# Kernel tuning notes

Measured on AMD Instinct MI355X. Metric: run time of the kernel, lower is better.

## Reference

```python
import jax, jax.numpy as jnp
import numpy as np

H = 12          # num heads
D = 768         # embed dim
HD = D // H     # head dim
SCALE = HD ** -0.5
NEG = -(3.0 ** 39)  # matches torch's triu(1) * -3.0**39 mask value


def setup_inputs() -> dict:
    key = jax.random.key(0)
    ks = jax.random.split(key, 9)
    B, S = 4, 1024
    lim = 1.0 / np.sqrt(D)
    def lin(k):
        kw, kb = jax.random.split(k)
        W = jax.random.uniform(kw, (D, D), jnp.float32, -lim, lim)  # [out,in]
        b = jax.random.uniform(kb, (D,), jnp.float32, -lim, lim)
        return W, b
    Wq, bq = lin(ks[0]); Wk, bk = lin(ks[1]); Wv, bv = lin(ks[2]); Wo, bo = lin(ks[3])
    hidden_states = jax.random.normal(ks[4], (B, S, D), jnp.float32)
    return {"hidden_states": hidden_states,
            "Wq": Wq, "bq": bq, "Wk": Wk, "bk": bk,
            "Wv": Wv, "bv": bv, "Wo": Wo, "bo": bo}


def reference(hidden_states, Wq, bq, Wk, bk, Wv, bv, Wo, bo):
    B, S, _ = hidden_states.shape
    split = lambda x: x.reshape(B, S, H, HD).transpose(0, 2, 1, 3)  # [B,H,S,HD]
    q = split(hidden_states @ Wq.T + bq) * SCALE
    k = split(hidden_states @ Wk.T + bk)
    v = split(hidden_states @ Wv.T + bv)
    scores = jnp.einsum('bhqd,bhkd->bhqk', q, k)
    causal_mask = jnp.triu(jnp.full((S, S), NEG, hidden_states.dtype), k=1)
    scores = scores + causal_mask  # broadcast over [B,H]
    probs = jax.nn.softmax(scores, axis=-1)
    out = jnp.einsum('bhqk,bhkd->bhqd', probs, v)
    out = out.transpose(0, 2, 1, 3).reshape(B, S, H * HD)
    return out @ Wo.T + bo
```

## Files before the change

### kernel.cpp

```cpp
#include <hip/hip_runtime.h>

#define NH 12
#define DM 768
#define HD 64
#define BB 4
#define SS 1024
#define MTOT (BB*SS)
#define ATT_SCALE 0.125f
#define NEGMASK (-4.0525551530189755e18f)

typedef __attribute__((ext_vector_type(8))) short short8;
typedef __attribute__((ext_vector_type(4))) float floatx4;
typedef __attribute__((ext_vector_type(4))) unsigned short ushort4v;

__device__ __forceinline__ float bf2f(unsigned short u){
    union { unsigned int i; float f; } x; x.i = ((unsigned int)u) << 16; return x.f;
}
__device__ __forceinline__ unsigned short f2bf(float f){
    union { float f; unsigned int i; } x; x.f = f;
    unsigned int i = x.i;
    return (unsigned short)((i + 0x7FFFu + ((i >> 16) & 1u)) >> 16);
}

#define XQ4 (MTOT*DM/4)
#define WQ4 (DM*DM/4)

__global__ __launch_bounds__(256) void convert_bf16(
    const float* __restrict__ X,
    const float* __restrict__ Wq, const float* __restrict__ Wk,
    const float* __restrict__ Wv, const float* __restrict__ Wo,
    unsigned short* __restrict__ Xb,
    unsigned short* __restrict__ Wqb, unsigned short* __restrict__ Wkb,
    unsigned short* __restrict__ Wvb, unsigned short* __restrict__ Wob)
{
    const int idx = blockIdx.x * 256 + threadIdx.x;
    const float* s; unsigned short* d; int off;
    if (idx < XQ4) { s = X; d = Xb; off = idx; }
    else {
        const int r = idx - XQ4;
        const int wsel = r / WQ4;
        off = r - wsel * WQ4;
        s = (wsel==0)?Wq:(wsel==1)?Wk:(wsel==2)?Wv:Wo;
        d = (wsel==0)?Wqb:(wsel==1)?Wkb:(wsel==2)?Wvb:Wob;
    }
    const float4 v = ((const float4*)s)[off];
    ushort4v o;
    o[0] = f2bf(v.x); o[1] = f2bf(v.y); o[2] = f2bf(v.z); o[3] = f2bf(v.w);
    ((ushort4v*)d)[off] = o;
}

__device__ __forceinline__ void gemm_stage64(
    const unsigned short* __restrict__ A,
    const unsigned short* __restrict__ Bm,
    int m0, int n0, int k0, int w, int lane,
    unsigned short* __restrict__ As,
    unsigned short* __restrict__ Bs)
{
    const int rsub = lane >> 3;
    const int cc   = (lane & 7) ^ rsub;
    #pragma unroll
    for (int j = 0; j < 4; ++j) {
        const int rb = w*32 + j*8;
        __builtin_amdgcn_global_load_lds(
            (const __attribute__((address_space(1))) unsigned int*)
                (A + (size_t)(m0 + rb + rsub) * DM + k0 + cc*8),
            (__attribute__((address_space(3))) unsigned int*)(As + rb*64),
            16, 0, 0);
    }
    #pragma unroll
    for (int j = 0; j < 2; ++j) {
        const int rb = w*16 + j*8;
        __builtin_amdgcn_global_load_lds(
            (const __attribute__((address_space(1))) unsigned int*)
                (Bm + (size_t)(n0 + rb + rsub) * DM + k0 + cc*8),
            (__attribute__((address_space(3))) unsigned int*)(Bs + rb*64),
            16, 0, 0);
    }
}

__device__ __forceinline__ void gemm_compute64(
    const unsigned short* __restrict__ As,
    const unsigned short* __restrict__ Bs,
    int wr, int wc, int c, int g, floatx4 (&acc)[4][2])
{
    #pragma unroll
    for (int st = 0; st < 2; ++st) {
        const int chunk = ((g + 4*st) ^ (c & 7)) * 8;
        short8 af[4], bfr[2];
        #pragma unroll
        for (int mi = 0; mi < 4; ++mi)
            af[mi] = *(const short8*)(As + (wr*64 + mi*16 + c)*64 + chunk);
        #pragma unroll
        for (int ni = 0; ni < 2; ++ni)
            bfr[ni] = *(const short8*)(Bs + (wc*32 + ni*16 + c)*64 + chunk);
        #pragma unroll
        for (int mi = 0; mi < 4; ++mi)
            #pragma unroll
            for (int ni = 0; ni < 2; ++ni)
                acc[mi][ni] = __builtin_amdgcn_mfma_f32_16x16x32_bf16(
                    af[mi], bfr[ni], acc[mi][ni], 0, 0, 0);
    }
}

__global__ __launch_bounds__(256) void qkv_mfma(
    const unsigned short* __restrict__ Xb,
    const unsigned short* __restrict__ Wqkv,
    const float* __restrict__ bq, const float* __restrict__ bk,
    const float* __restrict__ bv,
    unsigned short* __restrict__ qout,
    unsigned short* __restrict__ kout,
    unsigned short* __restrict__ vout)
{
    const int bx = blockIdx.x;
    const int which = bx / 12;
    const int np0 = (bx % 12) * 64;
    const int n0 = bx * 64;
    const int m0 = blockIdx.y * 128;

    const float* bias = (which==0) ? bq : (which==1) ? bk : bv;
    const float scl = (which==0) ? ATT_SCALE : 1.0f;

    __shared__ unsigned short As[128*64];
    __shared__ unsigned short Bs[64*64];

    const int t = threadIdx.x;
    const int w = t >> 6, lane = t & 63;
    const int c = lane & 15, g = lane >> 4;
    const int wr = w >> 1, wc = w & 1;

    floatx4 acc[4][2] = {};

    for (int kt = 0; kt < 12; ++kt) {
        __syncthreads();
        gemm_stage64(Xb, Wqkv, m0, n0, kt*64, w, lane, As, Bs);
        __syncthreads();
        gemm_compute64(As, Bs, wr, wc, c, g, acc);
    }

    #pragma unroll
    for (int mi = 0; mi < 4; ++mi) {
        #pragma unroll
        for (int r = 0; r < 4; ++r) {
            const int m = m0 + wr*64 + mi*16 + g*4 + r;
            const int b = m >> 10, s = m & 1023;
            #pragma unroll
            for (int ni = 0; ni < 2; ++ni) {
                const int np = np0 + wc*32 + ni*16 + c;
                const int h = np >> 6, hd = np & 63;
                const float val = (acc[mi][ni][r] + bias[np]) * scl;
                if (which == 2)
                    vout[(((size_t)(b*NH + h))*HD + hd)*SS + s] = f2bf(val);
                else if (which == 1)
                    kout[(((size_t)(b*NH + h))*SS + s)*HD + hd] = f2bf(val);
                else
                    qout[(((size_t)(b*NH + h))*SS + s)*HD + hd] = f2bf(val);
            }
        }
    }
}

__device__ __forceinline__ void stage_tile(
    const unsigned short* __restrict__ Kp,
    const unsigned short* __restrict__ VTp,
    int k0, int w, int lane,
    unsigned short* __restrict__ Ks,
    unsigned short* __restrict__ Vs)
{
    const int rsub = lane >> 3;
    const int cc   = (lane & 7) ^ rsub;
    #pragma unroll
    for (int j = 0; j < 2; ++j) {
        const int r = w*16 + j*8 + rsub;
        __builtin_amdgcn_global_load_lds(
            (const __attribute__((address_space(1))) unsigned int*)
                (Kp + (size_t)(k0 + r) * HD + cc*8),
            (__attribute__((address_space(3))) unsigned int*)
                (Ks + (w*16 + j*8) * HD),
            16, 0, 0);
        __builtin_amdgcn_global_load_lds(
            (const __attribute__((address_space(1))) unsigned int*)
                (VTp + (size_t)r * SS + k0 + cc*8),
            (__attribute__((address_space(3))) unsigned int*)
                (Vs + (w*16 + j*8) * HD),
            16, 0, 0);
    }
}

__device__ __forceinline__ void attn_process_tile(
    const unsigned short* __restrict__ Ks,
    const unsigned short* __restrict__ Vs,
    const short8 (&qf)[2],
    int k0, bool islast, int qg, int c, int g,
    float& m_c, float& l_c, floatx4 (&Oacc)[4],
    unsigned short* __restrict__ Pl)
{
    floatx4 S[4] = {};
    #pragma unroll
    for (int nf = 0; nf < 4; ++nf) {
        const int row = nf*16 + c;
        #pragma unroll
        for (int st = 0; st < 2; ++st) {
            const short8 kf = *(const short8*)(Ks + row*HD + (((g + 4*st) ^ (c & 7)) * 8));
            S[nf] = __builtin_amdgcn_mfma_f32_16x16x32_bf16(kf, qf[st], S[nf], 0, 0, 0);
        }
    }

    if (islast) {
        #pragma unroll
        for (int nf = 0; nf < 4; ++nf) {
            #pragma unroll
            for (int r = 0; r < 4; ++r) {
                const int key = k0 + nf*16 + g*4 + r;
                if (key > qg) S[nf][r] += NEGMASK;
            }
        }
    }

    float mx = -INFINITY;
    #pragma unroll
    for (int nf = 0; nf < 4; ++nf)
        #pragma unroll
        for (int r = 0; r < 4; ++r) mx = fmaxf(mx, S[nf][r]);
    mx = fmaxf(mx, __shfl_xor(mx, 16, 64));
    mx = fmaxf(mx, __shfl_xor(mx, 32, 64));
    const float mnew = fmaxf(m_c, mx);
    const float alpha = __expf(m_c - mnew);
    float sum = 0.0f;
    #pragma unroll
    for (int nf = 0; nf < 4; ++nf)
        #pragma unroll
        for (int r = 0; r < 4; ++r) {
            const float p = __expf(S[nf][r] - mnew);
            S[nf][r] = p;
            sum += p;
        }
    sum += __shfl_xor(sum, 16, 64);
    sum += __shfl_xor(sum, 32, 64);
    l_c = l_c * alpha + sum;
    m_c = mnew;
    #pragma unroll
    for (int nf = 0; nf < 4; ++nf)
        #pragma unroll
        for (int r = 0; r < 4; ++r) Oacc[nf][r] *= alpha;

    #pragma unroll
    for (int nf = 0; nf < 4; ++nf) {
        ushort4v p4;
        #pragma unroll
        for (int r = 0; r < 4; ++r) p4[r] = f2bf(S[nf][r]);
        *(ushort4v*)(Pl + c*72 + nf*16 + g*4) = p4;
    }

    #pragma unroll
    for (int st = 0; st < 2; ++st) {
        const short8 pf = *(const short8*)(Pl + c * 72 + g*8 + 32*st);
        #pragma unroll
        for (int nf = 0; nf < 4; ++nf) {
            const int row = nf*16 + c;
            const short8 vf = *(const short8*)(Vs + row*HD + (((g + 4*st) ^ (c & 7)) * 8));
            Oacc[nf] = __builtin_amdgcn_mfma_f32_16x16x32_bf16(vf, pf, Oacc[nf], 0, 0, 0);
        }
    }
}

__global__ __launch_bounds__(256) void attn_mfma(
    const unsigned short* __restrict__ Q,
    const unsigned short* __restrict__ K,
    const unsigned short* __restrict__ VT,
    unsigned short* __restrict__ O)
{
    const int idx = blockIdx.x;
    const int bh  = idx % 48;
    const int z   = 15 - (idx / 48);
    const int q0  = z * 64;

    const unsigned short* Qp  = Q  + (size_t)bh * SS * HD;
    const unsigned short* Kp  = K  + (size_t)bh * SS * HD;
    const unsigned short* VTp = VT + (size_t)bh * HD * SS;

    __shared__ unsigned short Ks[2][64*HD];
    __shared__ unsigned short Vs[2][64*HD];
    __shared__ unsigned short Pl[4][16*72];

    const int t    = threadIdx.x;
    const int w    = t >> 6;
    const int lane = t & 63;
    const int c    = lane & 15;
    const int g    = lane >> 4;
    const int qg   = q0 + w*16 + c;

    short8 qf[2];
    #pragma unroll
    for (int st = 0; st < 2; ++st)
        qf[st] = *(const short8*)(Qp + (size_t)qg * HD + g*8 + 32*st);

    floatx4 Oacc[4] = {};
    float m_c = -INFINITY, l_c = 0.0f;

    const int ntile = z + 1;

    stage_tile(Kp, VTp, 0, w, lane, Ks[0], Vs[0]);
    __syncthreads();

    for (int kt = 0; kt < ntile; ++kt) {
        const int cur = kt & 1;
        if (kt + 1 < ntile)
            stage_tile(Kp, VTp, (kt+1)*64, w, lane, Ks[cur^1], Vs[cur^1]);
        attn_process_tile(Ks[cur], Vs[cur], qf, kt*64, kt == ntile-1,
                          qg, c, g, m_c, l_c, Oacc, Pl[w]);
        if (kt + 1 < ntile)
            __syncthreads();
    }

    const int b = bh / NH, h = bh % NH;
    const float inv = 1.0f / l_c;
    unsigned short* op = O + ((size_t)(b*SS + qg))*DM + h*HD;
    #pragma unroll
    for (int nf = 0; nf < 4; ++nf) {
        ushort4v o4;
        #pragma unroll
        for (int r = 0; r < 4; ++r) o4[r] = f2bf(Oacc[nf][r] * inv);
        *(ushort4v*)(op + nf*16 + g*4) = o4;
    }
}

__global__ __launch_bounds__(256) void out_mfma(
    const unsigned short* __restrict__ A,
    const unsigned short* __restrict__ Wb,
    const float* __restrict__ bias,
    float* __restrict__ outf)
{
    const int n0 = blockIdx.x * 64;
    const int m0 = blockIdx.y * 128;

    __shared__ unsigned short As[128*64];
    __shared__ unsigned short Bs[64*64];

    const int t = threadIdx.x;
    const int w = t >> 6, lane = t & 63;
    const int c = lane & 15, g = lane >> 4;
    const int wr = w >> 1, wc = w & 1;

    floatx4 acc[4][2] = {};

    for (int kt = 0; kt < 12; ++kt) {
        __syncthreads();
        gemm_stage64(A, Wb, m0, n0, kt*64, w, lane, As, Bs);
        __syncthreads();
        gemm_compute64(As, Bs, wr, wc, c, g, acc);
    }

    #pragma unroll
    for (int mi = 0; mi < 4; ++mi) {
        #pragma unroll
        for (int r = 0; r < 4; ++r) {
            const int m = m0 + wr*64 + mi*16 + g*4 + r;
            #pragma unroll
            for (int ni = 0; ni < 2; ++ni) {
                const int n = n0 + wc*32 + ni*16 + c;
                outf[(size_t)m * DM + n] = acc[mi][ni][r] + bias[n];
            }
        }
    }
}

extern "C" void kernel_launch(void* const* d_in, const int* in_sizes, int n_in,
                              void* d_out, int out_size, void* d_ws, size_t ws_size,
                              hipStream_t stream) {
    const float* X  = (const float*)d_in[0];
    const float* Wq = (const float*)d_in[1];
    const float* bq = (const float*)d_in[2];
    const float* Wk = (const float*)d_in[3];
    const float* bk = (const float*)d_in[4];
    const float* Wv = (const float*)d_in[5];
    const float* bv = (const float*)d_in[6];
    const float* Wo = (const float*)d_in[7];
    const float* bo = (const float*)d_in[8];
    float* out = (float*)d_out;

    const size_t elems = (size_t)MTOT * DM;
    const size_t welems = (size_t)DM * DM;
    unsigned short* q    = (unsigned short*)d_ws;
    unsigned short* k    = q    + elems;
    unsigned short* vt   = k    + elems;
    unsigned short* attn = vt   + elems;
    unsigned short* xb   = attn + elems;
    unsigned short* wqb  = xb   + elems;
    unsigned short* wkb  = wqb  + welems;
    unsigned short* wvb  = wkb  + welems;
    unsigned short* wob  = wvb  + welems;

    convert_bf16<<<dim3((XQ4 + 4*WQ4) / 256), 256, 0, stream>>>(
        X, Wq, Wk, Wv, Wo, xb, wqb, wkb, wvb, wob);
    qkv_mfma<<<dim3(36, 32), 256, 0, stream>>>(
        xb, wqb, bq, bk, bv, q, k, vt);
    attn_mfma<<<dim3(768), 256, 0, stream>>>(q, k, vt, attn);
    out_mfma<<<dim3(12, 32), 256, 0, stream>>>(attn, wob, bo, out);
}
```

Measured before the change: 153.8 us.

## Process 128 queries per attention block, fold log2e into Q scale, use exp2

Each attention workgroup now handles 128 query rows, with each wave owning two 16-row query tiles, so every staged K/V tile feeds twice as many MFMAs. The log2(e) factor is folded into the Q scale and mask constant so the softmax can use exp2f, and probabilities are packed to bf16 by truncation instead of round-to-nearest. Waves skip tiles that lie entirely above their causal diagonal. The trade-off is half as many blocks (384), which lowers occupancy and parallelism, higher register pressure, and a small precision change from truncating P.

```diff
diff --git a/kernel.cpp b/kernel.cpp
--- a/kernel.cpp
+++ b/kernel.cpp
@@ -6,12 +6,13 @@
 #define BB 4
 #define SS 1024
 #define MTOT (BB*SS)
-#define ATT_SCALE 0.125f
-#define NEGMASK (-4.0525551530189755e18f)
+#define ATT_SCALE_L2E 0.18033688011112042f
+#define NEGMASK_L2E  (-5.846602e18f)
 
 typedef __attribute__((ext_vector_type(8))) short short8;
 typedef __attribute__((ext_vector_type(4))) float floatx4;
 typedef __attribute__((ext_vector_type(4))) unsigned short ushort4v;
+typedef __attribute__((ext_vector_type(2))) unsigned int uint2v;
 
 __device__ __forceinline__ float bf2f(unsigned short u){
     union { unsigned int i; float f; } x; x.i = ((unsigned int)u) << 16; return x.f;
@@ -20,6 +21,10 @@
     union { float f; unsigned int i; } x; x.f = f;
     unsigned int i = x.i;
     return (unsigned short)((i + 0x7FFFu + ((i >> 16) & 1u)) >> 16);
+}
+__device__ __forceinline__ unsigned int pack_trunc(float lo, float hi){
+    union { float f; unsigned int i; } a, b; a.f = lo; b.f = hi;
+    return (b.i & 0xffff0000u) | (a.i >> 16);
 }
 
 #define XQ4 (MTOT*DM/4)
@@ -118,7 +123,7 @@
     const int m0 = blockIdx.y * 128;
 
     const float* bias = (which==0) ? bq : (which==1) ? bk : bv;
-    const float scl = (which==0) ? ATT_SCALE : 1.0f;
+    const float scl = (which==0) ? ATT_SCALE_L2E : 1.0f;
 
     __shared__ unsigned short As[128*64];
     __shared__ unsigned short Bs[64*64];
@@ -189,76 +194,90 @@
 __device__ __forceinline__ void attn_process_tile(
     const unsigned short* __restrict__ Ks,
     const unsigned short* __restrict__ Vs,
-    const short8 (&qf)[2],
-    int k0, bool islast, int qg, int c, int g,
-    float& m_c, float& l_c, floatx4 (&Oacc)[4],
+    const short8 (&qf)[2][2],
+    int k0, int qw0, int c, int g,
+    float (&m_c)[2], float (&l_c)[2], floatx4 (&Oacc)[4][2],
     unsigned short* __restrict__ Pl)
 {
-    floatx4 S[4] = {};
+    floatx4 S[4][2] = {};
     #pragma unroll
     for (int nf = 0; nf < 4; ++nf) {
         const int row = nf*16 + c;
         #pragma unroll
         for (int st = 0; st < 2; ++st) {
             const short8 kf = *(const short8*)(Ks + row*HD + (((g + 4*st) ^ (c & 7)) * 8));
-            S[nf] = __builtin_amdgcn_mfma_f32_16x16x32_bf16(kf, qf[st], S[nf], 0, 0, 0);
-        }
-    }
-
-    if (islast) {
+            #pragma unroll
+            for (int qt = 0; qt < 2; ++qt)
+                S[nf][qt] = __builtin_amdgcn_mfma_f32_16x16x32_bf16(kf, qf[qt][st], S[nf][qt], 0, 0, 0);
+        }
+    }
+
+    if (k0 + 63 > qw0) {
+        #pragma unroll
+        for (int qt = 0; qt < 2; ++qt) {
+            const int qg = qw0 + 16*qt + c;
+            #pragma unroll
+            for (int nf = 0; nf < 4; ++nf) {
+                #pragma unroll
+                for (int r = 0; r < 4; ++r) {
+                    const int key = k0 + nf*16 + g*4 + r;
+                    if (key > qg) S[nf][qt][r] += NEGMASK_L2E;
+                }
+            }
+        }
+    }
+
+    #pragma unroll
+    for (int qt = 0; qt < 2; ++qt) {
+        float mx = -INFINITY;
+        #pragma unroll
+        for (int nf = 0; nf < 4; ++nf)
+            #pragma unroll
+            for (int r = 0; r < 4; ++r) mx = fmaxf(mx, S[nf][qt][r]);
+        mx = fmaxf(mx, __shfl_xor(mx, 16, 64));
+        mx = fmaxf(mx, __shfl_xor(mx, 32, 64));
+        const float mnew = fmaxf(m_c[qt], mx);
+        const float alpha = exp2f(m_c[qt] - mnew);
+        float sum = 0.0f;
+        #pragma unroll
+        for (int nf = 0; nf < 4; ++nf)
+            #pragma unroll
+            for (int r = 0; r < 4; ++r) {
+                const float p = exp2f(S[nf][qt][r] - mnew);
+                S[nf][qt][r] = p;
+                sum += p;
+            }
+        sum += __shfl_xor(sum, 16, 64);
+        sum += __shfl_xor(sum, 32, 64);
+        l_c[qt] = l_c[qt] * alpha + sum;
+        m_c[qt] = mnew;
+        #pragma unroll
+        for (int nf = 0; nf < 4; ++nf)
+            #pragma unroll
+            for (int r = 0; r < 4; ++r) Oacc[nf][qt][r] *= alpha;
+
         #pragma unroll
         for (int nf = 0; nf < 4; ++nf) {
-            #pragma unroll
-            for (int r = 0; r < 4; ++r) {
-                const int key = k0 + nf*16 + g*4 + r;
-                if (key > qg) S[nf][r] += NEGMASK;
-            }
-        }
-    }
-
-    float mx = -INFINITY;
-    #pragma unroll
-    for (int nf = 0; nf < 4; ++nf)
-        #pragma unroll
-        for (int r = 0; r < 4; ++r) mx = fmaxf(mx, S[nf][r]);
-    mx = fmaxf(mx, __shfl_xor(mx, 16, 64));
-    mx = fmaxf(mx, __shfl_xor(mx, 32, 64));
-    const float mnew = fmaxf(m_c, mx);
-    const float alpha = __expf(m_c - mnew);
-    float sum = 0.0f;
-    #pragma unroll
-    for (int nf = 0; nf < 4; ++nf)
-        #pragma unroll
-        for (int r = 0; r < 4; ++r) {
-            const float p = __expf(S[nf][r] - mnew);
-            S[nf][r] = p;
-            sum += p;
-        }
-    sum += __shfl_xor(sum, 16, 64);
-    sum += __shfl_xor(sum, 32, 64);
-    l_c = l_c * alpha + sum;
-    m_c = mnew;
-    #pragma unroll
-    for (int nf = 0; nf < 4; ++nf)
-        #pragma unroll
-        for (int r = 0; r < 4; ++r) Oacc[nf][r] *= alpha;
-
-    #pragma unroll
-    for (int nf = 0; nf < 4; ++nf) {
-        ushort4v p4;
-        #pragma unroll
-        for (int r = 0; r < 4; ++r) p4[r] = f2bf(S[nf][r]);
-        *(ushort4v*)(Pl + c*72 + nf*16 + g*4) = p4;
+            uint2v u;
+            u[0] = pack_trunc(S[nf][qt][0], S[nf][qt][1]);
+            u[1] = pack_trunc(S[nf][qt][2], S[nf][qt][3]);
+            *(uint2v*)(Pl + (16*qt + c)*72 + nf*16 + g*4) = u;
+        }
     }
 
     #pragma unroll
     for (int st = 0; st < 2; ++st) {
-        const short8 pf = *(const short8*)(Pl + c * 72 + g*8 + 32*st);
+        short8 pf[2];
+        #pragma unroll
+        for (int qt = 0; qt < 2; ++qt)
+            pf[qt] = *(const short8*)(Pl + (16*qt + c)*72 + g*8 + 32*st);
         #pragma unroll
         for (int nf = 0; nf < 4; ++nf) {
             const int row = nf*16 + c;
             const short8 vf = *(const short8*)(Vs + row*HD + (((g + 4*st) ^ (c & 7)) * 8));
-            Oacc[nf] = __builtin_amdgcn_mfma_f32_16x16x32_bf16(vf, pf, Oacc[nf], 0, 0, 0);
+            #pragma unroll
+            for (int qt = 0; qt < 2; ++qt)
+                Oacc[nf][qt] = __builtin_amdgcn_mfma_f32_16x16x32_bf16(vf, pf[qt], Oacc[nf][qt], 0, 0, 0);
         }
     }
 }
@@ -271,8 +290,8 @@
 {
     const int idx = blockIdx.x;
     const int bh  = idx % 48;
-    const int z   = 15 - (idx / 48);
-    const int q0  = z * 64;
+    const int z   = 7 - (idx / 48);
+    const int q0  = z * 128;
 
     const unsigned short* Qp  = Q  + (size_t)bh * SS * HD;
     const unsigned short* Kp  = K  + (size_t)bh * SS * HD;
@@ -280,47 +299,54 @@
 
     __shared__ unsigned short Ks[2][64*HD];
     __shared__ unsigned short Vs[2][64*HD];
-    __shared__ unsigned short Pl[4][16*72];
+    __shared__ unsigned short Pl[4][32*72];
 
     const int t    = threadIdx.x;
     const int w    = t >> 6;
     const int lane = t & 63;
     const int c    = lane & 15;
     const int g    = lane >> 4;
-    const int qg   = q0 + w*16 + c;
-
-    short8 qf[2];
-    #pragma unroll
-    for (int st = 0; st < 2; ++st)
-        qf[st] = *(const short8*)(Qp + (size_t)qg * HD + g*8 + 32*st);
-
-    floatx4 Oacc[4] = {};
-    float m_c = -INFINITY, l_c = 0.0f;
-
-    const int ntile = z + 1;
+    const int qw0  = q0 + w*32;
+
+    short8 qf[2][2];
+    #pragma unroll
+    for (int qt = 0; qt < 2; ++qt)
+        #pragma unroll
+        for (int st = 0; st < 2; ++st)
+            qf[qt][st] = *(const short8*)(Qp + (size_t)(qw0 + 16*qt + c) * HD + g*8 + 32*st);
+
+    floatx4 Oacc[4][2] = {};
+    float m_c[2] = {-INFINITY, -INFINITY}, l_c[2] = {0.0f, 0.0f};
+
+    const int ntile = 2*z + 2;
 
     stage_tile(Kp, VTp, 0, w, lane, Ks[0], Vs[0]);
     __syncthreads();
 
     for (int kt = 0; kt < ntile; ++kt) {
         const int cur = kt & 1;
+        const int k0 = kt * 64;
         if (kt + 1 < ntile)
             stage_tile(Kp, VTp, (kt+1)*64, w, lane, Ks[cur^1], Vs[cur^1]);
-        attn_process_tile(Ks[cur], Vs[cur], qf, kt*64, kt == ntile-1,
-                          qg, c, g, m_c, l_c, Oacc, Pl[w]);
+        if (k0 <= qw0 + 31)
+            attn_process_tile(Ks[cur], Vs[cur], qf, k0, qw0,
+                              c, g, m_c, l_c, Oacc, Pl[w]);
         if (kt + 1 < ntile)
             __syncthreads();
     }
 
     const int b = bh / NH, h = bh % NH;
-    const float inv = 1.0f / l_c;
-    unsigned short* op = O + ((size_t)(b*SS + qg))*DM + h*HD;
-    #pragma unroll
-    for (int nf = 0; nf < 4; ++nf) {
-        ushort4v o4;
-        #pragma unroll
-        for (int r = 0; r < 4; ++r) o4[r] = f2bf(Oacc[nf][r] * inv);
-        *(ushort4v*)(op + nf*16 + g*4) = o4;
+    #pragma unroll
+    for (int qt = 0; qt < 2; ++qt) {
+        const float inv = 1.0f / l_c[qt];
+        unsigned short* op = O + ((size_t)(b*SS + qw0 + 16*qt + c))*DM + h*HD;
+        #pragma unroll
+        for (int nf = 0; nf < 4; ++nf) {
+            ushort4v o4;
+            #pragma unroll
+            for (int r = 0; r < 4; ++r) o4[r] = f2bf(Oacc[nf][qt][r] * inv);
+            *(ushort4v*)(op + nf*16 + g*4) = o4;
+        }
     }
 }
 
@@ -394,6 +420,6 @@
         X, Wq, Wk, Wv, Wo, xb, wqb, wkb, wvb, wob);
     qkv_mfma<<<dim3(36, 32), 256, 0, stream>>>(
         xb, wqb, bq, bk, bv, q, k, vt);
-    attn_mfma<<<dim3(768), 256, 0, stream>>>(q, k, vt, attn);
+    attn_mfma<<<dim3(384), 256, 0, stream>>>(q, k, vt, attn);
     out_mfma<<<dim3(12, 32), 256, 0, stream>>>(attn, wob, bo, out);
 }
```

Result: slower. 167.5 us (+8.9%).
